# Performance work log

Hardware: AMD Instinct MI355X
Metric: run time of the kernel (lower is better)

The kernel has to match this reference:

```python
import jax, jax.numpy as jnp
import numpy as np
from jax import lax

D_MODEL = 1024
D_INNER = 2048   # expand * d_model
D_STATE = 16
DT_RANK = 64     # ceil(d_model / 16)
D_CONV = 4
B, L = 2, 1024


def setup_inputs() -> dict:
    key = jax.random.key(0)
    ks = jax.random.split(key, 8)
    s = 0.02
    x = jax.random.normal(ks[0], (B, L, D_MODEL), dtype=jnp.float32)
    in_proj_w = jax.random.normal(ks[1], (2 * D_INNER, D_MODEL), dtype=jnp.float32) * s
    conv_w = jax.random.normal(ks[2], (D_INNER, D_CONV), dtype=jnp.float32) * s  # depthwise kernel
    conv_b = jax.random.normal(ks[3], (D_INNER,), dtype=jnp.float32) * s
    x_proj_w = jax.random.normal(ks[4], (DT_RANK + 2 * D_STATE, D_INNER), dtype=jnp.float32) * s
    dt_proj_w = jax.random.normal(ks[5], (D_INNER, DT_RANK), dtype=jnp.float32) * s
    dt_proj_b = jax.random.normal(ks[6], (D_INNER,), dtype=jnp.float32) * s
    A_log = jnp.log(jnp.broadcast_to(jnp.arange(1, D_STATE + 1, dtype=jnp.float32), (D_INNER, D_STATE)))
    D = jnp.ones((D_INNER,), dtype=jnp.float32)
    out_proj_w = jax.random.normal(ks[7], (D_MODEL, D_INNER), dtype=jnp.float32) * s
    return {"x": x, "in_proj_w": in_proj_w, "conv_w": conv_w, "conv_b": conv_b,
            "x_proj_w": x_proj_w, "dt_proj_w": dt_proj_w, "dt_proj_b": dt_proj_b,
            "A_log": A_log, "D": D, "out_proj_w": out_proj_w}


def _causal_depthwise_conv(x, conv_w, conv_b):
    # x: (B, L, d_inner); torch Conv1d(padding=d_conv-1) then [:, :, :L] == causal left pad
    Lx = x.shape[1]
    k = conv_w.shape[-1]
    xp = jnp.pad(x, ((0, 0), (k - 1, 0), (0, 0)))
    out = conv_b
    # small fixed kernel width (4): unrolled taps, fully vectorized over B,L,D
    out = sum(xp[:, i:i + Lx, :] * conv_w[:, i] for i in range(k)) + conv_b
    return out


def mamba_forward(x, in_proj_w, conv_w, conv_b, x_proj_w, dt_proj_w, dt_proj_b, A_log, D, out_proj_w):
    xz = x @ in_proj_w.T                       # (B, L, 2*d_inner)
    xi, z = xz[..., :D_INNER], xz[..., D_INNER:]
    xc = jax.nn.silu(_causal_depthwise_conv(xi, conv_w, conv_b))  # (B, L, d_inner)

    x_dbl = xc @ x_proj_w.T                    # (B, L, dt_rank + 2*d_state)
    dt = x_dbl[..., :DT_RANK]
    Bm = x_dbl[..., DT_RANK:DT_RANK + D_STATE]  # (B, L, N)
    Cm = x_dbl[..., DT_RANK + D_STATE:]         # (B, L, N)
    delta = jax.nn.softplus(dt @ dt_proj_w.T + dt_proj_b)  # (B, L, d_inner)

    A = -jnp.exp(A_log)                        # (d_inner, N)
    deltaA = jnp.exp(delta[..., None] * A)                           # (B, L, D, N)
    deltaBx = delta[..., None] * Bm[:, :, None, :] * xc[..., None]   # (B, L, D, N)

    def step(h, inp):
        dA, dBx, Ct = inp                      # (B,D,N), (B,D,N), (B,N)
        h = dA * h + dBx
        y = jnp.einsum('bdn,bn->bd', h, Ct)
        return h, y

    h0 = jnp.zeros((x.shape[0], D_INNER, D_STATE), dtype=x.dtype)
    _, ys = lax.scan(step, h0, (deltaA.transpose(1, 0, 2, 3),
                                deltaBx.transpose(1, 0, 2, 3),
                                Cm.transpose(1, 0, 2)))
    y = ys.transpose(1, 0, 2)                  # (B, L, d_inner)
    y = y + xc * D
    y = y * jax.nn.silu(z)
    return y @ out_proj_w.T                    # (B, L, d_model)


def reference(x, in_proj_w, conv_w, conv_b, x_proj_w, dt_proj_w, dt_proj_b, A_log, D, out_proj_w):
    return mamba_forward(x, in_proj_w, conv_w, conv_b, x_proj_w, dt_proj_w, dt_proj_b, A_log, D, out_proj_w)
```

## Files before the change

kernel.cpp:

```cpp
#include <hip/hip_runtime.h>
#include <hip/hip_bf16.h>
#include <cstdint>
#include <cstddef>

#define DMODEL 1024
#define DINNER 2048
#define NSTATE 16
#define DTRANK 64
#define BATCH 2
#define SEQ 1024
#define ROWS (BATCH*SEQ)
#define NCHUNK 16
#define CLEN (SEQ/NCHUNK)
#define KSPLIT 16

typedef __attribute__((ext_vector_type(8))) short short8;
typedef __attribute__((ext_vector_type(4))) float f32x4;

__device__ __forceinline__ float bf2f(__hip_bfloat16 h){ return __bfloat162float(h); }
__device__ __forceinline__ float sigmoidf_(float x){ return 1.0f/(1.0f + __expf(-x)); }

__device__ __forceinline__ void gld16(const void* g, void* l){
  __builtin_amdgcn_global_load_lds((const __attribute__((address_space(1))) void*)g,
                                   (__attribute__((address_space(3))) void*)l, 16, 0, 0);
}

__global__ void sniff_k(const unsigned short* __restrict__ xu, int* __restrict__ flag)
{
  int t = threadIdx.x;
  int cnt = 0;
  for (int i = t; i < 1024; i += 64) {
    unsigned short u = xu[i];
    int e = (u >> 7) & 0xFF;
    if (e >= 0x70 && e <= 0x86) cnt++;
  }
  for (int o = 32; o; o >>= 1) cnt += __shfl_down(cnt, o);
  if (t == 0) *flag = (cnt >= 768) ? 0 : 1;
}

struct CvtArgs {
  const void *s0,*s1,*s2,*s3,*s4,*s5,*s6,*s7,*s8,*s9;
  __hip_bfloat16 *xB,*inpB,*xprojB,*dtprojB,*outpB;
  float *cwF,*cbF,*dtbF,*alF,*DF;
  const int* flag;
};
#define CVT_C1 2097152
#define CVT_C2 6291456
#define CVT_C3 6299648
#define CVT_C4 6301696
#define CVT_C5 6498304
#define CVT_C6 6629376
#define CVT_C7 6631424
#define CVT_C8 6664192
#define CVT_C9 6666240
#define CVT_TOT 8763392

__device__ __forceinline__ float cvt_read(const void* s, int j, int fl){
  return fl ? ((const float*)s)[j] : bf2f(((const __hip_bfloat16*)s)[j]);
}

__global__ __launch_bounds__(256)
void convert_all_k(CvtArgs a)
{
  int i = blockIdx.x * 256 + threadIdx.x;
  if (i >= CVT_TOT) return;
  const int fl = *a.flag;
  if (i < CVT_C1)      a.xB[i]                = __float2bfloat16(cvt_read(a.s0, i, fl));
  else if (i < CVT_C2) a.inpB[i-CVT_C1]       = __float2bfloat16(cvt_read(a.s1, i-CVT_C1, fl));
  else if (i < CVT_C3) a.cwF[i-CVT_C2]        = cvt_read(a.s2, i-CVT_C2, fl);
  else if (i < CVT_C4) a.cbF[i-CVT_C3]        = cvt_read(a.s3, i-CVT_C3, fl);
  else if (i < CVT_C5) a.xprojB[i-CVT_C4]     = __float2bfloat16(cvt_read(a.s4, i-CVT_C4, fl));
  else if (i < CVT_C6) a.dtprojB[i-CVT_C5]    = __float2bfloat16(cvt_read(a.s5, i-CVT_C5, fl));
  else if (i < CVT_C7) a.dtbF[i-CVT_C6]       = cvt_read(a.s6, i-CVT_C6, fl);
  else if (i < CVT_C8) a.alF[i-CVT_C7]        = cvt_read(a.s7, i-CVT_C7, fl);
  else if (i < CVT_C9) a.DF[i-CVT_C8]         = cvt_read(a.s8, i-CVT_C8, fl);
  else                 a.outpB[i-CVT_C9]      = __float2bfloat16(cvt_read(a.s9, i-CVT_C9, fl));
}

template<int EPI>
__global__ __launch_bounds__(256)
void gemm_bt(const __hip_bfloat16* __restrict__ A,
             const __hip_bfloat16* __restrict__ W,
             int M, int N, int K, int ldC, int kchunk,
             float* __restrict__ outF,
             __hip_bfloat16* __restrict__ outH,
             const float* __restrict__ biasF,
             float* __restrict__ q0, float* __restrict__ q1,
             float* __restrict__ q2, float* __restrict__ q3)
{
  __shared__ alignas(16) __hip_bfloat16 As[128*32];
  __shared__ alignas(16) __hip_bfloat16 Ws[128*32];
  const int tid  = threadIdx.x;
  const int lane = tid & 63;
  const int wave = tid >> 6;
  const int wm = wave & 1, wn = wave >> 1;
  const int row0 = blockIdx.y * 128;
  const int col0 = blockIdx.x * 128;

  f32x4 acc[4][4] = {};

  const int e0 = tid, e1 = tid + 256;

  int kbeg = 0, kend = K;
  if (EPI == 5 || EPI == 6) { kbeg = blockIdx.z * kchunk; kend = kbeg + kchunk; }

  for (int k0 = kbeg; k0 < kend; k0 += 32) {
    {
      int r = e0 >> 2, ks = e0 & 3;
      gld16(A + (size_t)(row0 + r) * K + k0 + ks*8, (char*)As + (size_t)e0*16);
      r = e1 >> 2; ks = e1 & 3;
      gld16(A + (size_t)(row0 + r) * K + k0 + ks*8, (char*)As + (size_t)e1*16);
    }
    {
      int r = e0 >> 2, ks = e0 & 3;
      int rw = col0 + r; if (rw > N-1) rw = N-1;
      gld16(W + (size_t)rw * K + k0 + ks*8, (char*)Ws + (size_t)e0*16);
      r = e1 >> 2; ks = e1 & 3;
      rw = col0 + r; if (rw > N-1) rw = N-1;
      gld16(W + (size_t)rw * K + k0 + ks*8, (char*)Ws + (size_t)e1*16);
    }
    __syncthreads();

    const char* Ab = (const char*)As + ((wm*64 + (lane & 15)) * 64) + ((lane >> 4) * 16);
    const char* Wb = (const char*)Ws + ((wn*64 + (lane & 15)) * 64) + ((lane >> 4) * 16);
    short8 af[4], wf[4];
#pragma unroll
    for (int i = 0; i < 4; ++i) af[i] = *(const short8*)(Ab + i*16*64);
#pragma unroll
    for (int i = 0; i < 4; ++i) wf[i] = *(const short8*)(Wb + i*16*64);
#pragma unroll
    for (int mt = 0; mt < 4; ++mt)
#pragma unroll
      for (int nt = 0; nt < 4; ++nt)
        acc[mt][nt] = __builtin_amdgcn_mfma_f32_16x16x32_bf16(af[mt], wf[nt], acc[mt][nt], 0, 0, 0);
    __syncthreads();
  }

  const int mbase = row0 + wm*64 + ((lane >> 4) * 4);
  const int nbase = col0 + wn*64 + (lane & 15);

  float bv[4];
  if (EPI == 3) {
#pragma unroll
    for (int nt = 0; nt < 4; ++nt) bv[nt] = biasF[nbase + nt*16];
  }
  float* qz = nullptr;
  if (EPI == 6) qz = (blockIdx.z == 0) ? q0 : (blockIdx.z == 1) ? q1
                   : (blockIdx.z == 2) ? q2 : q3;

#pragma unroll
  for (int mt = 0; mt < 4; ++mt) {
#pragma unroll
    for (int nt = 0; nt < 4; ++nt) {
#pragma unroll
      for (int r = 0; r < 4; ++r) {
        int row = mbase + mt*16 + r;
        int col = nbase + nt*16;
        float v = acc[mt][nt][r];
        if (EPI == 0) {
          outF[(size_t)row * ldC + col] = v;
        } else if (EPI == 3) {
          v += bv[nt];
          float sp = fmaxf(v, 0.0f) + __logf(1.0f + __expf(-fabsf(v)));
          outF[(size_t)row * ldC + col] = sp;
        } else if (EPI == 4) {
          if (col < DINNER) {
            outH[(size_t)row * DINNER + col] = __float2bfloat16(v);
          } else {
            outF[(size_t)row * DINNER + (col - DINNER)] = v * sigmoidf_(v);
          }
        } else if (EPI == 5) {
          if (col < 96)
            outF[(size_t)blockIdx.z * (ROWS*96) + (size_t)row * 96 + col] = v;
        } else if (EPI == 6) {
          qz[(size_t)row * DMODEL + col] = v;
        }
      }
    }
  }
}

__global__ __launch_bounds__(256)
void reduce_xdbl_k(const float* __restrict__ part, float* __restrict__ xdbl,
                   __hip_bfloat16* __restrict__ dtH)
{
  int i = blockIdx.x * 256 + threadIdx.x;
  if (i >= ROWS*96) return;
  float s = 0.f;
#pragma unroll
  for (int kc = 0; kc < KSPLIT; ++kc) s += part[(size_t)kc*ROWS*96 + i];
  xdbl[i] = s;
  int row = i / 96, col = i - row*96;
  if (col < 64) dtH[(size_t)row*64 + col] = __float2bfloat16(s);
}

__global__ __launch_bounds__(256)
void reduce_out_k(const float* __restrict__ q0, const float* __restrict__ q1,
                  const float* __restrict__ q2, const float* __restrict__ q3,
                  float* __restrict__ out)
{
  int i = blockIdx.x * 256 + threadIdx.x;
  if (i >= ROWS*DMODEL) return;
  out[i] = (q0[i] + q1[i]) + (q2[i] + q3[i]);
}

__global__ __launch_bounds__(256)
void conv_silu_k(const __hip_bfloat16* __restrict__ xi,
                 const float* __restrict__ cw,
                 const float* __restrict__ cb,
                 __hip_bfloat16* __restrict__ xcH)
{
  int idx = blockIdx.x * 256 + threadIdx.x;
  if (idx >= ROWS * DINNER) return;
  int d  = idx & (DINNER - 1);
  int t  = (idx >> 11) & (SEQ - 1);
  int bt = idx >> 11;
  float acc = cb[d];
#pragma unroll
  for (int i = 0; i < 4; ++i) {
    int tt = t - 3 + i;
    if (tt >= 0) acc += cw[d*4 + i] * bf2f(xi[(size_t)(bt - 3 + i) * DINNER + d]);
  }
  float y = acc * sigmoidf_(acc);
  xcH[idx] = __float2bfloat16(y);
}

#define GSTEP 8

__global__ __launch_bounds__(256)
void stats_k(const float* __restrict__ delta,
             const __hip_bfloat16* __restrict__ xcH,
             const float* __restrict__ xdbl,
             const float* __restrict__ alF,
             float* __restrict__ Hc, float* __restrict__ Sd)
{
  __shared__ alignas(16) float Bs[CLEN*16];
  const int bid  = blockIdx.x;
  const int b    = bid >> 9;
  const int c    = (bid >> 5) & (NCHUNK-1);
  const int cg   = bid & 31;
  const int tid  = threadIdx.x;
  const int lane = tid & 63;
  const int wave = tid >> 6;
  const int sub  = lane & 3;
  const int ch   = (cg << 6) + (wave << 4) + (lane >> 2);

  const size_t rb = (size_t)b * SEQ + (size_t)c * CLEN;

  for (int i = tid; i < CLEN*16; i += 256) {
    int t = i >> 4, j = i & 15;
    Bs[i] = xdbl[(rb + t)*96 + 64 + j];
  }
  __syncthreads();

  float negA[4];
#pragma unroll
  for (int j = 0; j < 4; ++j) negA[j] = -__expf(alF[ch*NSTATE + sub*4 + j]);

  const float*          dp = delta + rb * DINNER + ch;
  const __hip_bfloat16* xp = xcH   + rb * DINNER + ch;

  float h0=0.f,h1=0.f,h2=0.f,h3=0.f, sd=0.f;
  float d0[GSTEP], x0[GSTEP], d1[GSTEP], x1[GSTEP];

#define PF1(D_,X_,T0) \
  _Pragma("unroll") \
  for (int u = 0; u < GSTEP; ++u) { \
    D_[u] = dp[(size_t)((T0)+u) * DINNER]; \
    X_[u] = bf2f(xp[(size_t)((T0)+u) * DINNER]); \
  }
#define ST1(D_,X_,T0) \
  _Pragma("unroll") \
  for (int u = 0; u < GSTEP; ++u) { \
    float d_ = D_[u]; \
    sd += d_; \
    float du = d_ * X_[u]; \
    f32x4 B4 = *(const f32x4*)&Bs[((T0)+u)*16 + sub*4]; \
    h0 = __expf(d_*negA[0])*h0 + du*B4.x; \
    h1 = __expf(d_*negA[1])*h1 + du*B4.y; \
    h2 = __expf(d_*negA[2])*h2 + du*B4.z; \
    h3 = __expf(d_*negA[3])*h3 + du*B4.w; \
  }

  PF1(d0, x0, 0)
  for (int t0 = 0; t0 < CLEN; t0 += 2*GSTEP) {
    PF1(d1, x1, t0 + GSTEP)
    ST1(d0, x0, t0)
    if (t0 + 2*GSTEP < CLEN) { PF1(d0, x0, t0 + 2*GSTEP) }
    ST1(d1, x1, t0 + GSTEP)
  }
#undef PF1
#undef ST1

  const size_t bc = (size_t)(b*NCHUNK + c);
  f32x4 hv = { h0, h1, h2, h3 };
  *(f32x4*)&Hc[(bc*DINNER + ch)*NSTATE + sub*4] = hv;
  if (sub == 0) Sd[bc*DINNER + ch] = sd;
}

__global__ __launch_bounds__(256)
void carry_k(const float* __restrict__ Hc, const float* __restrict__ Sd,
             const float* __restrict__ alF, float* __restrict__ hin)
{
  int i = blockIdx.x * 256 + threadIdx.x;
  int n  = i & (NSTATE-1);
  int ch = (i >> 4) & (DINNER-1);
  int b  = i >> 15;
  float negA = -__expf(alF[ch * NSTATE + n]);
  float h = 0.f;
#pragma unroll
  for (int c = 0; c < NCHUNK; ++c) {
    size_t bc = (size_t)(b*NCHUNK + c);
    hin[(bc*DINNER + ch)*NSTATE + n] = h;
    float P = __expf(negA * Sd[bc*DINNER + ch]);
    h = P * h + Hc[(bc*DINNER + ch)*NSTATE + n];
  }
}

__global__ __launch_bounds__(256)
void emit_k(const float* __restrict__ delta,
            const __hip_bfloat16* __restrict__ xcH,
            const float* __restrict__ xdbl,
            const float* __restrict__ zsF,
            const float* __restrict__ alF,
            const float* __restrict__ DF,
            const float* __restrict__ hin,
            __hip_bfloat16* __restrict__ yH)
{
  __shared__ alignas(16) float BCs[CLEN*32];
  const int bid  = blockIdx.x;
  const int b    = bid >> 9;
  const int c    = (bid >> 5) & (NCHUNK-1);
  const int cg   = bid & 31;
  const int tid  = threadIdx.x;
  const int lane = tid & 63;
  const int wave = tid >> 6;
  const int sub  = lane & 3;
  const int ch   = (cg << 6) + (wave << 4) + (lane >> 2);

  const size_t rb = (size_t)b * SEQ + (size_t)c * CLEN;

  for (int i = tid; i < CLEN*32; i += 256) {
    int t = i >> 5, j = i & 31;
    BCs[i] = xdbl[(rb + t)*96 + 64 + j];
  }
  __syncthreads();

  float negA[4];
#pragma unroll
  for (int j = 0; j < 4; ++j) negA[j] = -__expf(alF[ch*NSTATE + sub*4 + j]);
  const float Dch = DF[ch];

  const float*          dp = delta + rb * DINNER + ch;
  const __hip_bfloat16* xp = xcH   + rb * DINNER + ch;
  const float*          zp = zsF   + rb * DINNER + ch;
  __hip_bfloat16*       yp = yH    + rb * DINNER + ch;

  f32x4 hv = *(const f32x4*)&hin[((size_t)(b*NCHUNK + c)*DINNER + ch)*NSTATE + sub*4];
  float h0=hv.x, h1=hv.y, h2=hv.z, h3=hv.w;

  float d0[GSTEP], x0[GSTEP], z0[GSTEP], d1[GSTEP], x1[GSTEP], z1[GSTEP];

#define PF(D_,X_,Z_,T0) \
  _Pragma("unroll") \
  for (int u = 0; u < GSTEP; ++u) { \
    D_[u] = dp[(size_t)((T0)+u) * DINNER]; \
    X_[u] = bf2f(xp[(size_t)((T0)+u) * DINNER]); \
    Z_[u] = zp[(size_t)((T0)+u) * DINNER]; \
  }
#define STEPS(D_,X_,Z_,T0) \
  _Pragma("unroll") \
  for (int u = 0; u < GSTEP; ++u) { \
    float d_ = D_[u]; \
    float du = d_ * X_[u]; \
    f32x4 B4 = *(const f32x4*)&BCs[((T0)+u)*32 + sub*4]; \
    f32x4 C4 = *(const f32x4*)&BCs[((T0)+u)*32 + 16 + sub*4]; \
    h0 = __expf(d_*negA[0])*h0 + du*B4.x; \
    h1 = __expf(d_*negA[1])*h1 + du*B4.y; \
    h2 = __expf(d_*negA[2])*h2 + du*B4.z; \
    h3 = __expf(d_*negA[3])*h3 + du*B4.w; \
    float p = h0*C4.x + h1*C4.y + h2*C4.z + h3*C4.w; \
    p += __shfl_xor(p, 1); \
    p += __shfl_xor(p, 2); \
    if (sub == 0) { \
      float y = (p + X_[u] * Dch) * Z_[u]; \
      yp[(size_t)((T0)+u) * DINNER] = __float2bfloat16(y); \
    } \
  }

  PF(d0, x0, z0, 0)
  for (int t0 = 0; t0 < CLEN; t0 += 2*GSTEP) {
    PF(d1, x1, z1, t0 + GSTEP)
    STEPS(d0, x0, z0, t0)
    if (t0 + 2*GSTEP < CLEN) { PF(d0, x0, z0, t0 + 2*GSTEP) }
    STEPS(d1, x1, z1, t0 + GSTEP)
  }
#undef PF
#undef STEPS
}

extern "C" void kernel_launch(void* const* d_in, const int* in_sizes, int n_in,
                              void* d_out, int out_size, void* d_ws, size_t ws_size,
                              hipStream_t stream)
{
  float* out = (float*)d_out;
  char* ws = (char*)d_ws;
  const size_t MB = 1024*1024;

  int*            flag    = (int*)            (ws);
  float*          cwF     = (float*)          (ws + 1024);
  float*          cbF     = (float*)          (ws + 40*1024);
  float*          dtbF    = (float*)          (ws + 56*1024);
  float*          alF     = (float*)          (ws + 72*1024);
  float*          DF      = (float*)          (ws + 208*1024);
  float*          Sd      = (float*)          (ws + 256*1024);
  __hip_bfloat16* xB      = (__hip_bfloat16*) (ws + 1*MB);
  __hip_bfloat16* inpB    = (__hip_bfloat16*) (ws + 5*MB);
  __hip_bfloat16* xiB     = (__hip_bfloat16*) (ws + 13*MB);
  float*          part    = (float*)          (ws + 1*MB);
  float*          dlt     = (float*)          (ws + 1*MB);
  __hip_bfloat16* xprojB  = (__hip_bfloat16*) (ws + 21*MB);
  __hip_bfloat16* dtprojB = (__hip_bfloat16*) (ws + 21*MB + 512*1024);
  __hip_bfloat16* outpB   = (__hip_bfloat16*) (ws + 22*MB);
  float*          zsF     = (float*)          (ws + 26*MB);
  __hip_bfloat16* xcH     = (__hip_bfloat16*) (ws + 42*MB);
  float*          xdbl    = (float*)          (ws + 50*MB);
  __hip_bfloat16* dtH     = (__hip_bfloat16*) (ws + 51*MB);
  __hip_bfloat16* yH      = (__hip_bfloat16*) (ws + 52*MB);
  float*          Hc      = (float*)          (ws + 60*MB);
  float*          hin     = (float*)          (ws + 64*MB);
  float*          q0      = (float*)          (ws + 26*MB);
  float*          q1      = (float*)          (ws + 34*MB);
  float*          q2      = (float*)          (ws + 42*MB);
  float*          q3      = (float*)          (ws + 1*MB);

  dim3 blk(256);

  sniff_k<<<1, 64, 0, stream>>>((const unsigned short*)d_in[0], flag);
  CvtArgs ca = { d_in[0], d_in[1], d_in[2], d_in[3], d_in[4],
                 d_in[5], d_in[6], d_in[7], d_in[8], d_in[9],
                 xB, inpB, xprojB, dtprojB, outpB,
                 cwF, cbF, dtbF, alF, DF, flag };
  convert_all_k<<<CVT_TOT/256, blk, 0, stream>>>(ca);

  gemm_bt<4><<<dim3(4096/128, ROWS/128), blk, 0, stream>>>(
      xB, inpB, ROWS, 2*DINNER, DMODEL, 0, 0, zsF, xiB, nullptr,
      nullptr, nullptr, nullptr, nullptr);

  conv_silu_k<<<(ROWS*DINNER)/256, blk, 0, stream>>>(xiB, cwF, cbF, xcH);

  gemm_bt<5><<<dim3(1, ROWS/128, KSPLIT), blk, 0, stream>>>(
      xcH, xprojB, ROWS, 96, DINNER, 0, DINNER/KSPLIT, part, nullptr, nullptr,
      nullptr, nullptr, nullptr, nullptr);
  reduce_xdbl_k<<<(ROWS*96+255)/256, blk, 0, stream>>>(part, xdbl, dtH);

  gemm_bt<3><<<dim3(DINNER/128, ROWS/128), blk, 0, stream>>>(
      dtH, dtprojB, ROWS, DINNER, DTRANK, DINNER, 0, dlt, nullptr, dtbF,
      nullptr, nullptr, nullptr, nullptr);

  stats_k<<<BATCH*NCHUNK*32, blk, 0, stream>>>(dlt, xcH, xdbl, alF, Hc, Sd);
  carry_k<<<(BATCH*DINNER*NSTATE)/256, blk, 0, stream>>>(Hc, Sd, alF, hin);
  emit_k<<<BATCH*NCHUNK*32, blk, 0, stream>>>(dlt, xcH, xdbl, zsF, alF, DF, hin, yH);

  gemm_bt<6><<<dim3(DMODEL/128, ROWS/128, 4), blk, 0, stream>>>(
      yH, outpB, ROWS, DMODEL, DINNER, 0, DINNER/4, nullptr, nullptr, nullptr,
      q0, q1, q2, q3);
  reduce_out_k<<<(ROWS*DMODEL+255)/256, blk, 0, stream>>>(q0, q1, q2, q3, out);
}
```

Baseline: 268.1 us.

## Use K=64 swizzled GEMM tiles, atomic split-K output, fold dtype sniff into convert

The GEMM K-step grows from 32 to 64, using XOR-swizzled LDS layouts to avoid bank conflicts. Each stage therefore does twice as many MFMAs per barrier pair. The out-projection split-K now accumulates with float atomics into an output buffer that the convert kernel zeroes, which removes the four partial buffers and the reduce kernel. The separate dtype-sniff kernel is merged into the convert kernel, where every wave recomputes the flag, saving two launches. In exchange the GEMMs use double the LDS, and atomic accumulation makes summation order nondeterministic.

```diff
diff --git a/kernel.cpp b/kernel.cpp
--- a/kernel.cpp
+++ b/kernel.cpp
@@ -25,24 +25,11 @@
                                    (__attribute__((address_space(3))) void*)l, 16, 0, 0);
 }
 
-__global__ void sniff_k(const unsigned short* __restrict__ xu, int* __restrict__ flag)
-{
-  int t = threadIdx.x;
-  int cnt = 0;
-  for (int i = t; i < 1024; i += 64) {
-    unsigned short u = xu[i];
-    int e = (u >> 7) & 0xFF;
-    if (e >= 0x70 && e <= 0x86) cnt++;
-  }
-  for (int o = 32; o; o >>= 1) cnt += __shfl_down(cnt, o);
-  if (t == 0) *flag = (cnt >= 768) ? 0 : 1;
-}
-
 struct CvtArgs {
   const void *s0,*s1,*s2,*s3,*s4,*s5,*s6,*s7,*s8,*s9;
   __hip_bfloat16 *xB,*inpB,*xprojB,*dtprojB,*outpB;
   float *cwF,*cbF,*dtbF,*alF,*DF;
-  const int* flag;
+  float *outZ;
 };
 #define CVT_C1 2097152
 #define CVT_C2 6291456
@@ -63,8 +50,25 @@
 void convert_all_k(CvtArgs a)
 {
   int i = blockIdx.x * 256 + threadIdx.x;
+  int lane = threadIdx.x & 63;
+  const unsigned short* xu = (const unsigned short*)a.s0;
+  int cnt = 0;
+#pragma unroll
+  for (int j = 0; j < 16; ++j) {
+    unsigned short u = xu[lane*16 + j];
+    int e = (u >> 7) & 0xFF;
+    cnt += (e >= 0x70 && e <= 0x86) ? 1 : 0;
+  }
+#pragma unroll
+  for (int o = 32; o; o >>= 1) cnt += __shfl_xor(cnt, o);
+  const int fl = (cnt >= 768) ? 0 : 1;
+
+  if (blockIdx.x < 2048) {
+    f32x4 z = {0.f, 0.f, 0.f, 0.f};
+    ((f32x4*)a.outZ)[i] = z;
+  }
+
   if (i >= CVT_TOT) return;
-  const int fl = *a.flag;
   if (i < CVT_C1)      a.xB[i]                = __float2bfloat16(cvt_read(a.s0, i, fl));
   else if (i < CVT_C2) a.inpB[i-CVT_C1]       = __float2bfloat16(cvt_read(a.s1, i-CVT_C1, fl));
   else if (i < CVT_C3) a.cwF[i-CVT_C2]        = cvt_read(a.s2, i-CVT_C2, fl);
@@ -79,17 +83,15 @@
 
 template<int EPI>
 __global__ __launch_bounds__(256)
-void gemm_bt(const __hip_bfloat16* __restrict__ A,
-             const __hip_bfloat16* __restrict__ W,
-             int M, int N, int K, int ldC, int kchunk,
-             float* __restrict__ outF,
-             __hip_bfloat16* __restrict__ outH,
-             const float* __restrict__ biasF,
-             float* __restrict__ q0, float* __restrict__ q1,
-             float* __restrict__ q2, float* __restrict__ q3)
-{
-  __shared__ alignas(16) __hip_bfloat16 As[128*32];
-  __shared__ alignas(16) __hip_bfloat16 Ws[128*32];
+void gemm64(const __hip_bfloat16* __restrict__ A,
+            const __hip_bfloat16* __restrict__ W,
+            int M, int N, int K, int kchunk,
+            float* __restrict__ outF,
+            __hip_bfloat16* __restrict__ outH,
+            const float* __restrict__ biasF)
+{
+  __shared__ alignas(16) __hip_bfloat16 As[128*64];
+  __shared__ alignas(16) __hip_bfloat16 Ws[128*64];
   const int tid  = threadIdx.x;
   const int lane = tid & 63;
   const int wave = tid >> 6;
@@ -99,54 +101,57 @@
 
   f32x4 acc[4][4] = {};
 
-  const int e0 = tid, e1 = tid + 256;
-
   int kbeg = 0, kend = K;
   if (EPI == 5 || EPI == 6) { kbeg = blockIdx.z * kchunk; kend = kbeg + kchunk; }
 
-  for (int k0 = kbeg; k0 < kend; k0 += 32) {
-    {
-      int r = e0 >> 2, ks = e0 & 3;
-      gld16(A + (size_t)(row0 + r) * K + k0 + ks*8, (char*)As + (size_t)e0*16);
-      r = e1 >> 2; ks = e1 & 3;
-      gld16(A + (size_t)(row0 + r) * K + k0 + ks*8, (char*)As + (size_t)e1*16);
+  const int r16 = lane & 15, q = lane >> 4;
+  const int sx0 = ((q ^ (r16 & 7)) * 16);
+
+  for (int k0 = kbeg; k0 < kend; k0 += 64) {
+#pragma unroll
+    for (int j = 0; j < 4; ++j) {
+      int e = tid + j*256;
+      int r = e >> 3, g = e & 7;
+      int kc = ((g ^ (r & 7)) << 3);
+      gld16(A + (size_t)(row0 + r) * K + k0 + kc, (char*)As + (size_t)e*16);
     }
-    {
-      int r = e0 >> 2, ks = e0 & 3;
-      int rw = col0 + r; if (rw > N-1) rw = N-1;
-      gld16(W + (size_t)rw * K + k0 + ks*8, (char*)Ws + (size_t)e0*16);
-      r = e1 >> 2; ks = e1 & 3;
-      rw = col0 + r; if (rw > N-1) rw = N-1;
-      gld16(W + (size_t)rw * K + k0 + ks*8, (char*)Ws + (size_t)e1*16);
+#pragma unroll
+    for (int j = 0; j < 4; ++j) {
+      int e = tid + j*256;
+      int r = e >> 3, g = e & 7;
+      int kc = ((g ^ (r & 7)) << 3);
+      int rw = col0 + r; if (EPI == 5 && rw > N-1) rw = N-1;
+      gld16(W + (size_t)rw * K + k0 + kc, (char*)Ws + (size_t)e*16);
     }
     __syncthreads();
 
-    const char* Ab = (const char*)As + ((wm*64 + (lane & 15)) * 64) + ((lane >> 4) * 16);
-    const char* Wb = (const char*)Ws + ((wn*64 + (lane & 15)) * 64) + ((lane >> 4) * 16);
-    short8 af[4], wf[4];
-#pragma unroll
-    for (int i = 0; i < 4; ++i) af[i] = *(const short8*)(Ab + i*16*64);
-#pragma unroll
-    for (int i = 0; i < 4; ++i) wf[i] = *(const short8*)(Wb + i*16*64);
-#pragma unroll
-    for (int mt = 0; mt < 4; ++mt)
-#pragma unroll
-      for (int nt = 0; nt < 4; ++nt)
-        acc[mt][nt] = __builtin_amdgcn_mfma_f32_16x16x32_bf16(af[mt], wf[nt], acc[mt][nt], 0, 0, 0);
+    const char* Ab = (const char*)As + ((wm*64 + r16) * 128);
+    const char* Wb = (const char*)Ws + ((wn*64 + r16) * 128);
+#pragma unroll
+    for (int ksub = 0; ksub < 2; ++ksub) {
+      const int sx = sx0 ^ (ksub * 64);
+      short8 af[4], wf[4];
+#pragma unroll
+      for (int i = 0; i < 4; ++i) af[i] = *(const short8*)(Ab + i*16*128 + sx);
+#pragma unroll
+      for (int i = 0; i < 4; ++i) wf[i] = *(const short8*)(Wb + i*16*128 + sx);
+#pragma unroll
+      for (int mt = 0; mt < 4; ++mt)
+#pragma unroll
+        for (int nt = 0; nt < 4; ++nt)
+          acc[mt][nt] = __builtin_amdgcn_mfma_f32_16x16x32_bf16(af[mt], wf[nt], acc[mt][nt], 0, 0, 0);
+    }
     __syncthreads();
   }
 
-  const int mbase = row0 + wm*64 + ((lane >> 4) * 4);
-  const int nbase = col0 + wn*64 + (lane & 15);
+  const int mbase = row0 + wm*64 + (q * 4);
+  const int nbase = col0 + wn*64 + r16;
 
   float bv[4];
   if (EPI == 3) {
 #pragma unroll
     for (int nt = 0; nt < 4; ++nt) bv[nt] = biasF[nbase + nt*16];
   }
-  float* qz = nullptr;
-  if (EPI == 6) qz = (blockIdx.z == 0) ? q0 : (blockIdx.z == 1) ? q1
-                   : (blockIdx.z == 2) ? q2 : q3;
 
 #pragma unroll
   for (int mt = 0; mt < 4; ++mt) {
@@ -157,12 +162,10 @@
         int row = mbase + mt*16 + r;
         int col = nbase + nt*16;
         float v = acc[mt][nt][r];
-        if (EPI == 0) {
-          outF[(size_t)row * ldC + col] = v;
-        } else if (EPI == 3) {
+        if (EPI == 3) {
           v += bv[nt];
           float sp = fmaxf(v, 0.0f) + __logf(1.0f + __expf(-fabsf(v)));
-          outF[(size_t)row * ldC + col] = sp;
+          outF[(size_t)row * DINNER + col] = sp;
         } else if (EPI == 4) {
           if (col < DINNER) {
             outH[(size_t)row * DINNER + col] = __float2bfloat16(v);
@@ -173,7 +176,7 @@
           if (col < 96)
             outF[(size_t)blockIdx.z * (ROWS*96) + (size_t)row * 96 + col] = v;
         } else if (EPI == 6) {
-          qz[(size_t)row * DMODEL + col] = v;
+          unsafeAtomicAdd(&outF[(size_t)row * DMODEL + col], v);
         }
       }
     }
@@ -192,16 +195,6 @@
   xdbl[i] = s;
   int row = i / 96, col = i - row*96;
   if (col < 64) dtH[(size_t)row*64 + col] = __float2bfloat16(s);
-}
-
-__global__ __launch_bounds__(256)
-void reduce_out_k(const float* __restrict__ q0, const float* __restrict__ q1,
-                  const float* __restrict__ q2, const float* __restrict__ q3,
-                  float* __restrict__ out)
-{
-  int i = blockIdx.x * 256 + threadIdx.x;
-  if (i >= ROWS*DMODEL) return;
-  out[i] = (q0[i] + q1[i]) + (q2[i] + q3[i]);
 }
 
 __global__ __launch_bounds__(256)
@@ -407,7 +400,6 @@
   char* ws = (char*)d_ws;
   const size_t MB = 1024*1024;
 
-  int*            flag    = (int*)            (ws);
   float*          cwF     = (float*)          (ws + 1024);
   float*          cbF     = (float*)          (ws + 40*1024);
   float*          dtbF    = (float*)          (ws + 56*1024);
@@ -429,41 +421,31 @@
   __hip_bfloat16* yH      = (__hip_bfloat16*) (ws + 52*MB);
   float*          Hc      = (float*)          (ws + 60*MB);
   float*          hin     = (float*)          (ws + 64*MB);
-  float*          q0      = (float*)          (ws + 26*MB);
-  float*          q1      = (float*)          (ws + 34*MB);
-  float*          q2      = (float*)          (ws + 42*MB);
-  float*          q3      = (float*)          (ws + 1*MB);
 
   dim3 blk(256);
 
-  sniff_k<<<1, 64, 0, stream>>>((const unsigned short*)d_in[0], flag);
   CvtArgs ca = { d_in[0], d_in[1], d_in[2], d_in[3], d_in[4],
                  d_in[5], d_in[6], d_in[7], d_in[8], d_in[9],
                  xB, inpB, xprojB, dtprojB, outpB,
-                 cwF, cbF, dtbF, alF, DF, flag };
+                 cwF, cbF, dtbF, alF, DF, out };
   convert_all_k<<<CVT_TOT/256, blk, 0, stream>>>(ca);
 
-  gemm_bt<4><<<dim3(4096/128, ROWS/128), blk, 0, stream>>>(
-      xB, inpB, ROWS, 2*DINNER, DMODEL, 0, 0, zsF, xiB, nullptr,
-      nullptr, nullptr, nullptr, nullptr);
+  gemm64<4><<<dim3(4096/128, ROWS/128), blk, 0, stream>>>(
+      xB, inpB, ROWS, 2*DINNER, DMODEL, 0, zsF, xiB, nullptr);
 
   conv_silu_k<<<(ROWS*DINNER)/256, blk, 0, stream>>>(xiB, cwF, cbF, xcH);
 
-  gemm_bt<5><<<dim3(1, ROWS/128, KSPLIT), blk, 0, stream>>>(
-      xcH, xprojB, ROWS, 96, DINNER, 0, DINNER/KSPLIT, part, nullptr, nullptr,
-      nullptr, nullptr, nullptr, nullptr);
+  gemm64<5><<<dim3(1, ROWS/128, KSPLIT), blk, 0, stream>>>(
+      xcH, xprojB, ROWS, 96, DINNER, DINNER/KSPLIT, part, nullptr, nullptr);
   reduce_xdbl_k<<<(ROWS*96+255)/256, blk, 0, stream>>>(part, xdbl, dtH);
 
-  gemm_bt<3><<<dim3(DINNER/128, ROWS/128), blk, 0, stream>>>(
-      dtH, dtprojB, ROWS, DINNER, DTRANK, DINNER, 0, dlt, nullptr, dtbF,
-      nullptr, nullptr, nullptr, nullptr);
+  gemm64<3><<<dim3(DINNER/128, ROWS/128), blk, 0, stream>>>(
+      dtH, dtprojB, ROWS, DINNER, DTRANK, 0, dlt, nullptr, dtbF);
 
   stats_k<<<BATCH*NCHUNK*32, blk, 0, stream>>>(dlt, xcH, xdbl, alF, Hc, Sd);
   carry_k<<<(BATCH*DINNER*NSTATE)/256, blk, 0, stream>>>(Hc, Sd, alF, hin);
   emit_k<<<BATCH*NCHUNK*32, blk, 0, stream>>>(dlt, xcH, xdbl, zsF, alF, DF, hin, yH);
 
-  gemm_bt<6><<<dim3(DMODEL/128, ROWS/128, 4), blk, 0, stream>>>(
-      yH, outpB, ROWS, DMODEL, DINNER, 0, DINNER/4, nullptr, nullptr, nullptr,
-      q0, q1, q2, q3);
-  reduce_out_k<<<(ROWS*DMODEL+255)/256, blk, 0, stream>>>(q0, q1, q2, q3, out);
-}
+  gemm64<6><<<dim3(DMODEL/128, ROWS/128, 4), blk, 0, stream>>>(
+      yH, outpB, ROWS, DMODEL, DINNER, DINNER/4, out, nullptr, nullptr);
+}
```

Result: slower. 281.5 us (+5.0%).
